# Kernel optimization log

Hardware: AMD Instinct MI355X
Metric: run time of the kernel (lower is better)

Reference implementation:

```python
import jax, jax.numpy as jnp
import numpy as np

B, T, D, U = 32, 512, 256, 1024

def setup_inputs() -> dict:
    key = jax.random.key(0)
    ks = jax.random.split(key, 5)
    return {
        "X_vecs": jax.random.normal(ks[0], (B, D), dtype=jnp.float32),
        "X_ts": jax.random.normal(ks[1], (B, T, D), dtype=jnp.float32),
        "mat_A_0": jax.random.normal(ks[2], (D, U), dtype=jnp.float32) * (1.0 / np.sqrt(D)),
        "vec_b_0": jnp.zeros((1, U), dtype=jnp.float32),
        "mat_A_s": jax.random.normal(ks[3], (D, U), dtype=jnp.float32) * (1.0 / np.sqrt(D)),
        "vec_b_s": jnp.zeros((1, U), dtype=jnp.float32),
        "mat_W_d": jax.random.normal(ks[4], (D, U), dtype=jnp.float32) * (1.0 / np.sqrt(D)),
        "vec_b_d": jnp.zeros((1, U), dtype=jnp.float32),
    }

def reference(X_vecs, X_ts, mat_A_0, vec_b_0, mat_A_s, vec_b_s, mat_W_d, vec_b_d):
    softsign = jax.nn.soft_sign  # x / (1 + |x|), the layer's main_activation
    # Learned initial state: H_0 = softsign(X_vecs @ A_0 + b_0)   [B, U]
    H0 = softsign(X_vecs @ mat_A_0 + vec_b_0)
    # Static per-step drive from the vector input (computed once, reused each t)
    drive = X_vecs @ mat_A_s + vec_b_s + vec_b_d  # [B, U]
    # Batched projection of the whole timeseries (one big GEMM instead of T small ones)
    XW = jnp.einsum('btd,du->btu', X_ts, mat_W_d)  # [B, T, U]
    def step(h, x_t):  # h: [B,U], x_t: [B,U]
        h_new = softsign(h + drive + x_t)
        return h_new, h_new
    _, outs = jax.lax.scan(step, H0, jnp.swapaxes(XW, 0, 1))  # outs: [T, B, U]
    return jnp.swapaxes(outs, 0, 1)  # return_sequences=True -> [B, T, U]
```

## Files before the change

### kernel.cpp

```cpp
#include <hip/hip_runtime.h>

#define B_DIM 32
#define T_DIM 512
#define D_DIM 256
#define U_DIM 1024
#define M_DIM (B_DIM * T_DIM)

typedef __bf16 bf16_t;
typedef bf16_t bf16x8 __attribute__((ext_vector_type(8)));
typedef float f32x4 __attribute__((ext_vector_type(4)));

__device__ __forceinline__ float ssign(float z) {
    return z * __builtin_amdgcn_rcpf(1.0f + __builtin_fabsf(z));
}

__global__ __launch_bounds__(256) void xcast(const float* __restrict__ X,
                                             bf16_t* __restrict__ Xb) {
    const int i = (blockIdx.x * 256 + threadIdx.x) * 8;
    const float4 a = *(const float4*)(X + i);
    const float4 b = *(const float4*)(X + i + 4);
    bf16x8 p;
    p[0]=(bf16_t)a.x; p[1]=(bf16_t)a.y; p[2]=(bf16_t)a.z; p[3]=(bf16_t)a.w;
    p[4]=(bf16_t)b.x; p[5]=(bf16_t)b.y; p[6]=(bf16_t)b.z; p[7]=(bf16_t)b.w;
    *(bf16x8*)(Xb + i) = p;
}

__global__ __launch_bounds__(256) void transpose_w(const float* __restrict__ Wd,
                                                   bf16_t* __restrict__ Wt) {
    __shared__ float tile[64][65];
    const int tx = threadIdx.x & 63;
    const int ty = threadIdx.x >> 6;
    const int n0 = blockIdx.x * 64;
    const int k0 = blockIdx.y * 64;
    #pragma unroll
    for (int rr = 0; rr < 16; ++rr) {
        const int kk = ty * 16 + rr;
        tile[kk][tx] = Wd[(size_t)(k0 + kk) * U_DIM + n0 + tx];
    }
    __syncthreads();
    #pragma unroll
    for (int rr = 0; rr < 16; ++rr) {
        const int nn = ty * 16 + rr;
        Wt[(size_t)(n0 + nn) * D_DIM + k0 + tx] = (bf16_t)tile[tx][nn];
    }
}

__global__ __launch_bounds__(64, 1) void fused_gemm_scan(
        const float* __restrict__ Xv, const float* __restrict__ A0,
        const float* __restrict__ b0, const float* __restrict__ As,
        const float* __restrict__ bs, const float* __restrict__ bd,
        const bf16_t* __restrict__ Xb, const bf16_t* __restrict__ Wt,
        float* __restrict__ out) {
    __shared__ float xvs[D_DIM];
    __shared__ float xwT[64 * 20];

    const int lane = threadIdx.x;
    const int b = blockIdx.x;
    const int u0 = blockIdx.y * 64;
    const int lm = lane & 15, q = lane >> 4;
    const int u = u0 + lane;

    ((float4*)xvs)[lane] = ((const float4*)(Xv + (size_t)b * D_DIM))[lane];
    __syncthreads();

    float h0a = 0.f, dra = 0.f;
    #pragma unroll 8
    for (int d = 0; d < D_DIM; ++d) {
        const float x = xvs[d];
        h0a = fmaf(x, A0[(size_t)d * U_DIM + u], h0a);
        dra = fmaf(x, As[(size_t)d * U_DIM + u], dra);
    }
    float h = ssign(h0a + b0[u]);
    const float drive = dra + bs[u] + bd[u];

    bf16x8 bW[4][8];
    #pragma unroll
    for (int n = 0; n < 4; ++n)
        #pragma unroll
        for (int kb = 0; kb < 8; ++kb)
            bW[n][kb] = *(const bf16x8*)(Wt + (size_t)(u0 + n * 16 + lm) * D_DIM + kb * 32 + q * 8);

    const bf16_t* xrow = Xb + ((size_t)b * T_DIM + lm) * D_DIM + q * 8;
    float* po = out + (size_t)b * T_DIM * U_DIM + u;

    bf16x8 aC[8], aN[8];
    #pragma unroll
    for (int kb = 0; kb < 8; ++kb) aC[kb] = *(const bf16x8*)(xrow + kb * 32);

    for (int c = 0; c < T_DIM / 16; ++c) {
        f32x4 acc[4];
        #pragma unroll
        for (int n = 0; n < 4; ++n) acc[n] = (f32x4){0.f, 0.f, 0.f, 0.f};

        #pragma unroll
        for (int kb = 0; kb < 8; ++kb)
            #pragma unroll
            for (int n = 0; n < 4; ++n)
                acc[n] = __builtin_amdgcn_mfma_f32_16x16x32_bf16(aC[kb], bW[n][kb], acc[n], 0, 0, 0);

        const int cn = (c < T_DIM / 16 - 1) ? c + 1 : c;
        const bf16_t* xn = xrow + (size_t)cn * 16 * D_DIM;
        #pragma unroll
        for (int kb = 0; kb < 8; ++kb) aN[kb] = *(const bf16x8*)(xn + kb * 32);

        #pragma unroll
        for (int n = 0; n < 4; ++n)
            *(f32x4*)&xwT[(n * 16 + lm) * 20 + q * 4] = acc[n];
        __syncthreads();

        #pragma unroll
        for (int j = 0; j < 4; ++j) {
            const f32x4 v = *(const f32x4*)&xwT[lane * 20 + j * 4];
            #pragma unroll
            for (int r = 0; r < 4; ++r) {
                h = ssign(h + drive + v[r]);
                po[(size_t)(c * 16 + j * 4 + r) * U_DIM] = h;
            }
        }
        __syncthreads();

        #pragma unroll
        for (int kb = 0; kb < 8; ++kb) aC[kb] = aN[kb];
    }
}

__global__ __launch_bounds__(256) void gemm_xw_f32(const float* __restrict__ Xts,
                                                   const float* __restrict__ Wd,
                                                   float* __restrict__ out) {
    __shared__ float xs[16 * D_DIM];
    const int tid = threadIdx.x;
    const int bt0 = blockIdx.y * 16;
    const int u = blockIdx.x * 256 + tid;
    const float4* src4 = (const float4*)(Xts + (size_t)bt0 * D_DIM);
    float4* xs4 = (float4*)xs;
    #pragma unroll
    for (int i = 0; i < 4; ++i) xs4[tid + 256 * i] = src4[tid + 256 * i];
    __syncthreads();
    float acc[16];
    #pragma unroll
    for (int r = 0; r < 16; ++r) acc[r] = 0.0f;
    const float* wp = Wd + u;
    for (int d0 = 0; d0 < D_DIM; d0 += 4) {
        const float w0 = wp[(size_t)(d0 + 0) * U_DIM];
        const float w1 = wp[(size_t)(d0 + 1) * U_DIM];
        const float w2 = wp[(size_t)(d0 + 2) * U_DIM];
        const float w3 = wp[(size_t)(d0 + 3) * U_DIM];
        #pragma unroll
        for (int r = 0; r < 16; ++r) {
            const float4 xvv = *(const float4*)&xs[r * D_DIM + d0];
            acc[r] = fmaf(xvv.x, w0, acc[r]);
            acc[r] = fmaf(xvv.y, w1, acc[r]);
            acc[r] = fmaf(xvv.z, w2, acc[r]);
            acc[r] = fmaf(xvv.w, w3, acc[r]);
        }
    }
    #pragma unroll
    for (int r = 0; r < 16; ++r)
        out[(size_t)(bt0 + r) * U_DIM + u] = acc[r];
}

__global__ __launch_bounds__(256) void scan_old(const float* __restrict__ Xv,
                                                const float* __restrict__ A0,
                                                const float* __restrict__ b0,
                                                const float* __restrict__ As,
                                                const float* __restrict__ bs,
                                                const float* __restrict__ bd,
                                                float* __restrict__ out) {
    __shared__ float xv[D_DIM];
    const int tid = threadIdx.x;
    const int b = blockIdx.y;
    const int u = blockIdx.x * 256 + tid;
    xv[tid] = Xv[(size_t)b * D_DIM + tid];
    __syncthreads();
    float a0 = 0.0f, asum = 0.0f;
    #pragma unroll 4
    for (int d = 0; d < D_DIM; ++d) {
        const float x = xv[d];
        a0   = fmaf(x, A0[(size_t)d * U_DIM + u], a0);
        asum = fmaf(x, As[(size_t)d * U_DIM + u], asum);
    }
    a0 += b0[u];
    const float drive = asum + bs[u] + bd[u];
    float h = ssign(a0);
    float* po = out + (size_t)b * T_DIM * U_DIM + u;
    float buf[8];
    #pragma unroll
    for (int i = 0; i < 8; ++i) buf[i] = po[(size_t)i * U_DIM];
    for (int t = 0; t < T_DIM; t += 8) {
        #pragma unroll
        for (int i = 0; i < 8; ++i) {
            const float x = buf[i];
            const int tn = t + i + 8;
            if (tn < T_DIM) buf[i] = po[(size_t)tn * U_DIM];
            h = ssign(h + drive + x);
            po[(size_t)(t + i) * U_DIM] = h;
        }
    }
}

extern "C" void kernel_launch(void* const* d_in, const int* in_sizes, int n_in,
                              void* d_out, int out_size, void* d_ws, size_t ws_size,
                              hipStream_t stream) {
    const float* Xv  = (const float*)d_in[0];
    const float* Xts = (const float*)d_in[1];
    const float* A0  = (const float*)d_in[2];
    const float* b0  = (const float*)d_in[3];
    const float* As  = (const float*)d_in[4];
    const float* bs  = (const float*)d_in[5];
    const float* Wd  = (const float*)d_in[6];
    const float* bd  = (const float*)d_in[7];
    float* out = (float*)d_out;

    const size_t OFF_XB = 1u << 20;
    const size_t NEED   = 16u << 20;

    if (ws_size >= NEED) {
        bf16_t* Wt = (bf16_t*)d_ws;
        bf16_t* Xb = (bf16_t*)((char*)d_ws + OFF_XB);
        transpose_w<<<dim3(U_DIM / 64, D_DIM / 64), dim3(256), 0, stream>>>(Wd, Wt);
        xcast<<<dim3(M_DIM * D_DIM / (256 * 8)), dim3(256), 0, stream>>>(Xts, Xb);
        fused_gemm_scan<<<dim3(B_DIM, U_DIM / 64), dim3(64), 0, stream>>>(
            Xv, A0, b0, As, bs, bd, Xb, Wt, out);
    } else {
        gemm_xw_f32<<<dim3(U_DIM / 256, M_DIM / 16), dim3(256), 0, stream>>>(Xts, Wd, out);
        scan_old<<<dim3(U_DIM / 256, B_DIM), dim3(256), 0, stream>>>(Xv, A0, b0, As, bs, bd, out);
    }
}
```

Measured before the change: 135.7 us.

## Double-buffer MFMA and scan stages and merge prep kernels into one launch

```diff
diff --git a/kernel.cpp b/kernel.cpp
--- a/kernel.cpp
+++ b/kernel.cpp
@@ -14,45 +14,47 @@
     return z * __builtin_amdgcn_rcpf(1.0f + __builtin_fabsf(z));
 }
 
-__global__ __launch_bounds__(256) void xcast(const float* __restrict__ X,
-                                             bf16_t* __restrict__ Xb) {
-    const int i = (blockIdx.x * 256 + threadIdx.x) * 8;
-    const float4 a = *(const float4*)(X + i);
-    const float4 b = *(const float4*)(X + i + 4);
-    bf16x8 p;
-    p[0]=(bf16_t)a.x; p[1]=(bf16_t)a.y; p[2]=(bf16_t)a.z; p[3]=(bf16_t)a.w;
-    p[4]=(bf16_t)b.x; p[5]=(bf16_t)b.y; p[6]=(bf16_t)b.z; p[7]=(bf16_t)b.w;
-    *(bf16x8*)(Xb + i) = p;
-}
-
-__global__ __launch_bounds__(256) void transpose_w(const float* __restrict__ Wd,
-                                                   bf16_t* __restrict__ Wt) {
-    __shared__ float tile[64][65];
-    const int tx = threadIdx.x & 63;
-    const int ty = threadIdx.x >> 6;
-    const int n0 = blockIdx.x * 64;
-    const int k0 = blockIdx.y * 64;
-    #pragma unroll
-    for (int rr = 0; rr < 16; ++rr) {
-        const int kk = ty * 16 + rr;
-        tile[kk][tx] = Wd[(size_t)(k0 + kk) * U_DIM + n0 + tx];
-    }
-    __syncthreads();
-    #pragma unroll
-    for (int rr = 0; rr < 16; ++rr) {
-        const int nn = ty * 16 + rr;
-        Wt[(size_t)(n0 + nn) * D_DIM + k0 + tx] = (bf16_t)tile[tx][nn];
-    }
-}
-
-__global__ __launch_bounds__(64, 1) void fused_gemm_scan(
+__global__ __launch_bounds__(256) void prep(const float* __restrict__ Wd,
+                                            bf16_t* __restrict__ Wt,
+                                            const float* __restrict__ X,
+                                            bf16_t* __restrict__ Xb) {
+    const int bid = blockIdx.x;
+    if (bid < 64) {
+        __shared__ float tile[64][65];
+        const int tx = threadIdx.x & 63;
+        const int ty = threadIdx.x >> 6;
+        const int n0 = (bid & 15) * 64;
+        const int k0 = (bid >> 4) * 64;
+        #pragma unroll
+        for (int rr = 0; rr < 16; ++rr) {
+            const int kk = ty * 16 + rr;
+            tile[kk][tx] = Wd[(size_t)(k0 + kk) * U_DIM + n0 + tx];
+        }
+        __syncthreads();
+        #pragma unroll
+        for (int rr = 0; rr < 16; ++rr) {
+            const int nn = ty * 16 + rr;
+            Wt[(size_t)(n0 + nn) * D_DIM + k0 + tx] = (bf16_t)tile[tx][nn];
+        }
+    } else {
+        const int i = ((bid - 64) * 256 + threadIdx.x) * 8;
+        const float4 a = *(const float4*)(X + i);
+        const float4 b = *(const float4*)(X + i + 4);
+        bf16x8 p;
+        p[0]=(bf16_t)a.x; p[1]=(bf16_t)a.y; p[2]=(bf16_t)a.z; p[3]=(bf16_t)a.w;
+        p[4]=(bf16_t)b.x; p[5]=(bf16_t)b.y; p[6]=(bf16_t)b.z; p[7]=(bf16_t)b.w;
+        *(bf16x8*)(Xb + i) = p;
+    }
+}
+
+__global__ __launch_bounds__(64, 1) void fused2(
         const float* __restrict__ Xv, const float* __restrict__ A0,
         const float* __restrict__ b0, const float* __restrict__ As,
         const float* __restrict__ bs, const float* __restrict__ bd,
         const bf16_t* __restrict__ Xb, const bf16_t* __restrict__ Wt,
         float* __restrict__ out) {
     __shared__ float xvs[D_DIM];
-    __shared__ float xwT[64 * 20];
+    __shared__ float xwT[2][64 * 20];
 
     const int lane = threadIdx.x;
     const int b = blockIdx.x;
@@ -60,9 +62,24 @@
     const int lm = lane & 15, q = lane >> 4;
     const int u = u0 + lane;
 
+    const bf16_t* xrow = Xb + ((size_t)b * T_DIM + lm) * D_DIM + q * 8;
+    float* po = out + (size_t)b * T_DIM * U_DIM + u;
+
+    bf16x8 aE[8], aO[8];
+    #pragma unroll
+    for (int kb = 0; kb < 8; ++kb) aE[kb] = *(const bf16x8*)(xrow + kb * 32);
+    #pragma unroll
+    for (int kb = 0; kb < 8; ++kb) aO[kb] = *(const bf16x8*)(xrow + (size_t)16 * D_DIM + kb * 32);
+
+    bf16x8 bW[4][8];
+    #pragma unroll
+    for (int n = 0; n < 4; ++n)
+        #pragma unroll
+        for (int kb = 0; kb < 8; ++kb)
+            bW[n][kb] = *(const bf16x8*)(Wt + (size_t)(u0 + n * 16 + lm) * D_DIM + kb * 32 + q * 8);
+
     ((float4*)xvs)[lane] = ((const float4*)(Xv + (size_t)b * D_DIM))[lane];
     __syncthreads();
-
     float h0a = 0.f, dra = 0.f;
     #pragma unroll 8
     for (int d = 0; d < D_DIM; ++d) {
@@ -73,55 +90,77 @@
     float h = ssign(h0a + b0[u]);
     const float drive = dra + bs[u] + bd[u];
 
-    bf16x8 bW[4][8];
-    #pragma unroll
-    for (int n = 0; n < 4; ++n)
-        #pragma unroll
-        for (int kb = 0; kb < 8; ++kb)
-            bW[n][kb] = *(const bf16x8*)(Wt + (size_t)(u0 + n * 16 + lm) * D_DIM + kb * 32 + q * 8);
-
-    const bf16_t* xrow = Xb + ((size_t)b * T_DIM + lm) * D_DIM + q * 8;
-    float* po = out + (size_t)b * T_DIM * U_DIM + u;
-
-    bf16x8 aC[8], aN[8];
-    #pragma unroll
-    for (int kb = 0; kb < 8; ++kb) aC[kb] = *(const bf16x8*)(xrow + kb * 32);
-
-    for (int c = 0; c < T_DIM / 16; ++c) {
-        f32x4 acc[4];
-        #pragma unroll
-        for (int n = 0; n < 4; ++n) acc[n] = (f32x4){0.f, 0.f, 0.f, 0.f};
-
-        #pragma unroll
-        for (int kb = 0; kb < 8; ++kb)
-            #pragma unroll
-            for (int n = 0; n < 4; ++n)
-                acc[n] = __builtin_amdgcn_mfma_f32_16x16x32_bf16(aC[kb], bW[n][kb], acc[n], 0, 0, 0);
-
-        const int cn = (c < T_DIM / 16 - 1) ? c + 1 : c;
-        const bf16_t* xn = xrow + (size_t)cn * 16 * D_DIM;
-        #pragma unroll
-        for (int kb = 0; kb < 8; ++kb) aN[kb] = *(const bf16x8*)(xn + kb * 32);
-
-        #pragma unroll
-        for (int n = 0; n < 4; ++n)
-            *(f32x4*)&xwT[(n * 16 + lm) * 20 + q * 4] = acc[n];
-        __syncthreads();
-
-        #pragma unroll
-        for (int j = 0; j < 4; ++j) {
-            const f32x4 v = *(const f32x4*)&xwT[lane * 20 + j * 4];
-            #pragma unroll
-            for (int r = 0; r < 4; ++r) {
-                h = ssign(h + drive + v[r]);
-                po[(size_t)(c * 16 + j * 4 + r) * U_DIM] = h;
-            }
-        }
-        __syncthreads();
-
-        #pragma unroll
-        for (int kb = 0; kb < 8; ++kb) aC[kb] = aN[kb];
-    }
+#define DO_MFMA(ACC, AF)                                                            \
+    {                                                                               \
+        _Pragma("unroll")                                                           \
+        for (int kb = 0; kb < 8; ++kb) {                                            \
+            _Pragma("unroll")                                                       \
+            for (int n = 0; n < 4; ++n)                                             \
+                ACC[n] = __builtin_amdgcn_mfma_f32_16x16x32_bf16(AF[kb], bW[n][kb], \
+                                                                 ACC[n], 0, 0, 0);  \
+        }                                                                           \
+    }
+
+#define LOAD_A(DST, CH)                                                             \
+    {                                                                               \
+        const bf16_t* xp_ = xrow + (size_t)(CH) * 16 * D_DIM;                       \
+        _Pragma("unroll")                                                           \
+        for (int kb = 0; kb < 8; ++kb) DST[kb] = *(const bf16x8*)(xp_ + kb * 32);   \
+    }
+
+#define STASH(ACC, BUF)                                                             \
+    {                                                                               \
+        _Pragma("unroll")                                                           \
+        for (int n = 0; n < 4; ++n)                                                 \
+            *(f32x4*)&xwT[BUF][(n * 16 + lm) * 20 + q * 4] = ACC[n];                \
+    }
+
+#define SCAN16(BUF, CBASE)                                                          \
+    {                                                                               \
+        const f32x4 v0 = *(const f32x4*)&xwT[BUF][lane * 20 + 0];                   \
+        const f32x4 v1 = *(const f32x4*)&xwT[BUF][lane * 20 + 4];                   \
+        const f32x4 v2 = *(const f32x4*)&xwT[BUF][lane * 20 + 8];                   \
+        const f32x4 v3 = *(const f32x4*)&xwT[BUF][lane * 20 + 12];                  \
+        float xp[16];                                                               \
+        _Pragma("unroll")                                                           \
+        for (int r = 0; r < 4; ++r) {                                               \
+            xp[r]      = drive + v0[r];                                             \
+            xp[4 + r]  = drive + v1[r];                                             \
+            xp[8 + r]  = drive + v2[r];                                             \
+            xp[12 + r] = drive + v3[r];                                             \
+        }                                                                           \
+        _Pragma("unroll")                                                           \
+        for (int j = 0; j < 16; ++j) {                                              \
+            h = ssign(h + xp[j]);                                                   \
+            po[(size_t)((CBASE) + j) * U_DIM] = h;                                  \
+        }                                                                           \
+    }
+
+    f32x4 accC[4], accN[4];
+    #pragma unroll
+    for (int n = 0; n < 4; ++n) accC[n] = (f32x4){0.f, 0.f, 0.f, 0.f};
+    DO_MFMA(accC, aE);
+
+    for (int cc = 0; cc < 32; cc += 2) {
+        STASH(accC, 0);
+        #pragma unroll
+        for (int n = 0; n < 4; ++n) accN[n] = (f32x4){0.f, 0.f, 0.f, 0.f};
+        DO_MFMA(accN, aO);
+        const int c2 = (cc + 2 < 32) ? cc + 2 : 31;
+        LOAD_A(aE, c2);
+        SCAN16(0, cc * 16);
+        STASH(accN, 1);
+        #pragma unroll
+        for (int n = 0; n < 4; ++n) accC[n] = (f32x4){0.f, 0.f, 0.f, 0.f};
+        DO_MFMA(accC, aE);
+        const int c3 = (cc + 3 < 32) ? cc + 3 : 31;
+        LOAD_A(aO, c3);
+        SCAN16(1, (cc + 1) * 16);
+    }
+#undef DO_MFMA
+#undef LOAD_A
+#undef STASH
+#undef SCAN16
 }
 
 __global__ __launch_bounds__(256) void gemm_xw_f32(const float* __restrict__ Xts,
@@ -217,9 +256,8 @@
     if (ws_size >= NEED) {
         bf16_t* Wt = (bf16_t*)d_ws;
         bf16_t* Xb = (bf16_t*)((char*)d_ws + OFF_XB);
-        transpose_w<<<dim3(U_DIM / 64, D_DIM / 64), dim3(256), 0, stream>>>(Wd, Wt);
-        xcast<<<dim3(M_DIM * D_DIM / (256 * 8)), dim3(256), 0, stream>>>(Xts, Xb);
-        fused_gemm_scan<<<dim3(B_DIM, U_DIM / 64), dim3(64), 0, stream>>>(
+        prep<<<dim3(64 + M_DIM * D_DIM / (256 * 8)), dim3(256), 0, stream>>>(Wd, Wt, Xts, Xb);
+        fused2<<<dim3(B_DIM, U_DIM / 64), dim3(64), 0, stream>>>(
             Xv, A0, b0, As, bs, bd, Xb, Wt, out);
     } else {
         gemm_xw_f32<<<dim3(U_DIM / 256, M_DIM / 16), dim3(256), 0, stream>>>(Xts, Wd, out);
```

New measurement: 129.5 us. 1.05x faster.
